# Kernel tuning notes

Measured on AMD Instinct MI355X. Metric: run time of the kernel, lower is better.

The kernel has to match this reference:

```python
import jax, jax.numpy as jnp
import numpy as np

N_OPS = 32
D_REASON = 128
TOP_K = 2
EPS = 1e-05
LEAK = 1e-05  # coefficient on the all-ops leak term


def setup_inputs() -> dict:
    key = jax.random.key(0)
    k1, k2, k3, k4 = jax.random.split(key, 4)
    B, S = 8, 2048
    x = jax.random.normal(k1, (B, S, D_REASON), dtype=jnp.float32)
    indices = jax.random.randint(k2, (B, S, TOP_K), 0, N_OPS, dtype=jnp.int64)
    weights = jax.random.uniform(k3, (B, S, TOP_K), dtype=jnp.float32)
    ops = 0.02 * jax.random.normal(k4, (N_OPS, D_REASON, D_REASON), dtype=jnp.float32)
    return {"x": x, "indices": indices, "weights": weights, "ops": ops}


def _ternary_effective(ops):
    # scale_n = clamp(mean|W_n|, 1e-5); q = STE ternary quantize; W_eff = q * scale
    scale = jnp.maximum(jnp.mean(jnp.abs(ops), axis=(1, 2)), EPS)  # (N,)
    q_hard = jnp.clip(jnp.round(ops / scale[:, None, None]), -1.0, 1.0)
    # STE: identity gradient w.r.t. ops through the quantizer
    q = ops + jax.lax.stop_gradient(q_hard - ops)
    return q * scale[:, None, None]  # (N, D, D)


def reference(x, indices, weights, ops):
    # x: (B,S,D); indices: (B,S,K) int; weights: (B,S,K); ops: (N,D,D)
    w_eff = _ternary_effective(ops)  # (N, D_out, D_in)
    # F.linear(x, W) = x @ W.T, for every op at once -> T: (B,S,N,D_out)
    T = jnp.einsum("bsd,nod->bsno", x, w_eff)
    total = T.sum(axis=2)  # sum over all ops, (B,S,D)
    # gather the selected top_k ops per token: (B,S,K,D)
    gathered = jnp.take_along_axis(T, indices[..., None].astype(jnp.int32), axis=2)
    routed = jnp.sum(weights[..., None] * gathered, axis=2)  # (B,S,D)
    return LEAK * total / N_OPS + routed
```

## Files before the change

kernel.cpp:

```cpp
#include <hip/hip_runtime.h>

#define N_OPS 32
#define D 128
#define MAT (D * D)
#define EPS 1e-5f
#define NTOK (8 * 2048)
#define NASSIGN (NTOK * 2)
#define CAP 40960
#define EXP_BLKS (CAP / 256)

typedef __attribute__((ext_vector_type(8))) short short8;
typedef __attribute__((ext_vector_type(4))) float f32x4;

__device__ inline unsigned short f2bf(float f) {
    unsigned int u = __float_as_uint(f);
    return (unsigned short)((u + 0x7FFF + ((u >> 16) & 1)) >> 16);
}
__device__ inline float bf2f(unsigned short h) {
    return __uint_as_float(((unsigned int)h) << 16);
}

__global__ __launch_bounds__(256) void k_prep(const float* __restrict__ ops,
                                              const int* __restrict__ idx,
                                              const float* __restrict__ x,
                                              float* __restrict__ scale,
                                              int* __restrict__ hist2,
                                              unsigned short* __restrict__ xb,
                                              unsigned short* __restrict__ wb) {
    if (blockIdx.x < N_OPS) {
        const int e = blockIdx.x;
        const float* W = ops + e * MAT;
        float s = 0.f;
        for (int i = threadIdx.x; i < MAT; i += 256) s += fabsf(W[i]);
        for (int off = 32; off; off >>= 1) s += __shfl_xor(s, off);
        __shared__ float red[4];
        __shared__ float s_scale;
        const int lane = threadIdx.x & 63, wid = threadIdx.x >> 6;
        if (lane == 0) red[wid] = s;
        __syncthreads();
        if (threadIdx.x == 0) {
            s_scale = fmaxf((red[0] + red[1] + red[2] + red[3]) / (float)MAT, EPS);
            scale[e] = s_scale;
        }
        __syncthreads();
        const float sc = s_scale;
#pragma unroll
        for (int it = 0; it < 8; ++it) {
            const int f = it * 256 + threadIdx.x;
            const int o = f >> 4, dc = f & 15;
            const float4* wp = (const float4*)(W + o * D + dc * 8);
            float4 a = wp[0], b = wp[1];
            float v[8] = {a.x, a.y, a.z, a.w, b.x, b.y, b.z, b.w};
            unsigned short q[8];
#pragma unroll
            for (int j = 0; j < 8; ++j) {
                float t = rintf(v[j] / sc);
                t = fminf(1.f, fmaxf(-1.f, t));
                q[j] = (t == 0.f) ? 0 : (t > 0.f ? 0x3F80 : 0xBF80);
            }
            ((short8*)wb)[e * 2048 + dc * 128 + o] = *(const short8*)q;
        }
    } else if (blockIdx.x < 64) {
        const int b = blockIdx.x - N_OPS;
        __shared__ int lh[N_OPS];
        if (threadIdx.x < N_OPS) lh[threadIdx.x] = 0;
        __syncthreads();
#pragma unroll
        for (int j = 0; j < 4; ++j)
            atomicAdd(&lh[idx[b * 1024 + j * 256 + threadIdx.x]], 1);
        __syncthreads();
        if (threadIdx.x < N_OPS) hist2[b * N_OPS + threadIdx.x] = lh[threadIdx.x];
    } else {
        const int gid = (blockIdx.x - 64) * 256 + threadIdx.x;
        const float4* xp = (const float4*)(x + (size_t)gid * 8);
        float4 a = xp[0], b = xp[1];
        unsigned short o[8] = {f2bf(a.x), f2bf(a.y), f2bf(a.z), f2bf(a.w),
                               f2bf(b.x), f2bf(b.y), f2bf(b.z), f2bf(b.w)};
        ((short8*)xb)[gid] = *(const short8*)o;
    }
}

__global__ __launch_bounds__(256) void k_scatter(const int* __restrict__ idx,
                                                 const int* __restrict__ hist2,
                                                 int* __restrict__ list,
                                                 int* __restrict__ slot_of) {
    const int b = blockIdx.x;
    __shared__ int hl[1024];
    __shared__ int stot[N_OPS];
    __shared__ int soff[N_OPS + 1];
    __shared__ int sbase[N_OPS];
    __shared__ int lh[N_OPS];
    for (int i = threadIdx.x; i < 1024; i += 256) hl[i] = hist2[i];
    if (threadIdx.x < N_OPS) lh[threadIdx.x] = 0;
    __syncthreads();
    if (threadIdx.x < N_OPS) {
        int t = 0;
        for (int b2 = 0; b2 < 32; ++b2) t += hl[b2 * N_OPS + threadIdx.x];
        stot[threadIdx.x] = t;
    }
    __syncthreads();
    if (threadIdx.x == 0) {
        int run = 0;
        for (int e = 0; e < N_OPS; ++e) { soff[e] = run; run += (stot[e] + 255) & ~255; }
        soff[N_OPS] = run;
    }
    __syncthreads();
    if (threadIdx.x < N_OPS) {
        const int e = threadIdx.x;
        int r = soff[e];
        for (int b2 = 0; b2 < b; ++b2) r += hl[b2 * N_OPS + e];
        sbase[e] = r;
    }
    __syncthreads();
#pragma unroll
    for (int j = 0; j < 4; ++j) {
        const int a = b * 1024 + j * 256 + threadIdx.x;
        const int e = idx[a];
        const int r = atomicAdd(&lh[e], 1);
        const int slot = sbase[e] + r;
        list[slot] = (e << 20) | a;
        slot_of[a] = slot;
    }
    for (int s = soff[b] + stot[b] + (int)threadIdx.x; s < soff[b + 1]; s += 256)
        list[s] = -1;
    if (b == 0)
        for (int s = soff[N_OPS] + (int)threadIdx.x; s < CAP; s += 256) list[s] = -1;
}

__global__ __launch_bounds__(256, 2) void k_mfma(const unsigned short* __restrict__ xb,
                                                 const int* __restrict__ list,
                                                 const unsigned short* __restrict__ wb,
                                                 const float* __restrict__ scale,
                                                 unsigned short* __restrict__ partial) {
    __shared__ short8 lB[2048];
    const int lane = threadIdx.x & 63;
    const int wv   = threadIdx.x >> 6;
    const int quad = lane >> 4;
    const int ncol = lane & 15;

    const int base = blockIdx.x * 256;
    const int v0 = list[base];
    if (v0 < 0) return;
    const int e = v0 >> 20;
    const short8* src = (const short8*)wb + e * 2048;
    const float sc = scale[e];

    for (int i = threadIdx.x; i < 2048; i += 256) lB[i] = src[i];
    __syncthreads();

    for (int g = 0; g < 4; ++g) {
        const int rowbase = base + g * 64 + wv * 16;
        const int v = list[rowbase + ncol];
        const int tok = (v < 0) ? 0 : ((v & 0xFFFFF) >> 1);
        const short8* Ap = (const short8*)(xb + (size_t)tok * D);

        f32x4 acc[8];
#pragma unroll
        for (int j = 0; j < 8; ++j) acc[j] = (f32x4){0.f, 0.f, 0.f, 0.f};

#pragma unroll
        for (int s = 0; s < 4; ++s) {
            const short8 a = Ap[s * 4 + quad];
            const short8* Bp = lB + (s * 4 + quad) * 128;
#pragma unroll
            for (int nt = 0; nt < 8; ++nt) {
                const short8 b = Bp[nt * 16 + ncol];
                acc[nt] = __builtin_amdgcn_mfma_f32_16x16x32_bf16(a, b, acc[nt], 0, 0, 0);
            }
        }
#pragma unroll
        for (int nt = 0; nt < 8; ++nt)
#pragma unroll
            for (int r = 0; r < 4; ++r)
                partial[(size_t)(rowbase + quad * 4 + r) * D + nt * 16 + ncol] =
                    f2bf(acc[nt][r] * sc);
    }
}

__global__ __launch_bounds__(256) void k_final(const unsigned short* __restrict__ partial,
                                               const int* __restrict__ slot_of,
                                               const float* __restrict__ wts,
                                               float* __restrict__ out) {
    const int lane = threadIdx.x & 63;
#pragma unroll
    for (int it = 0; it < 8; ++it) {
        const int t = __builtin_amdgcn_readfirstlane(
            blockIdx.x * 32 + it * 4 + (threadIdx.x >> 6));
        const int s0 = slot_of[2 * t], s1 = slot_of[2 * t + 1];
        const float w0 = wts[2 * t], w1 = wts[2 * t + 1];
        const unsigned int a0 = ((const unsigned int*)(partial + (size_t)s0 * D))[lane];
        const unsigned int a1 = ((const unsigned int*)(partial + (size_t)s1 * D))[lane];
        float2 o;
        o.x = w0 * bf2f((unsigned short)(a0 & 0xFFFF))
            + w1 * bf2f((unsigned short)(a1 & 0xFFFF));
        o.y = w0 * bf2f((unsigned short)(a0 >> 16))
            + w1 * bf2f((unsigned short)(a1 >> 16));
        ((float2*)out)[(size_t)t * 64 + lane] = o;
    }
}

extern "C" void kernel_launch(void* const* d_in, const int* in_sizes, int n_in,
                              void* d_out, int out_size, void* d_ws, size_t ws_size,
                              hipStream_t stream) {
    const float* x   = (const float*)d_in[0];
    const int*   idx = (const int*)  d_in[1];
    const float* wts = (const float*)d_in[2];
    const float* ops = (const float*)d_in[3];
    float* out = (float*)d_out;

    unsigned short* partial = (unsigned short*)d_ws;
    unsigned short* xb      = partial + (size_t)CAP * D;
    unsigned short* wb      = xb + (size_t)NTOK * D;
    float*          scale   = (float*)(wb + N_OPS * MAT);
    int*            hist2   = (int*)(scale + 32);
    int*            list    = hist2 + 1024;
    int*            slot_of = list + CAP;

    k_prep<<<1088, 256, 0, stream>>>(ops, idx, x, scale, hist2, xb, wb);
    k_scatter<<<32, 256, 0, stream>>>(idx, hist2, list, slot_of);
    k_mfma<<<EXP_BLKS, 256, 0, stream>>>(xb, list, wb, scale, partial);
    k_final<<<NTOK / 32, 256, 0, stream>>>(partial, slot_of, wts, out);
}
```

Baseline: 104.0 us.

## Fuse x bf16 conversion into MFMA and scatter partials by assignment index

Drops the separate pass that converts x to bf16 in k_prep. k_mfma now reads fp32 x rows directly and converts them in registers. k_mfma also writes each result row to a buffer indexed by assignment id rather than by slot, which removes the slot_of array so k_final reads contiguous rows. The aim is to save the x round-trip through memory and the indirection, at the cost of doubled x read bytes in the GEMM and scattered partial writes.

```diff
diff --git a/kernel.cpp b/kernel.cpp
--- a/kernel.cpp
+++ b/kernel.cpp
@@ -22,10 +22,8 @@
 
 __global__ __launch_bounds__(256) void k_prep(const float* __restrict__ ops,
                                               const int* __restrict__ idx,
-                                              const float* __restrict__ x,
                                               float* __restrict__ scale,
                                               int* __restrict__ hist2,
-                                              unsigned short* __restrict__ xb,
                                               unsigned short* __restrict__ wb) {
     if (blockIdx.x < N_OPS) {
         const int e = blockIdx.x;
@@ -60,7 +58,7 @@
             }
             ((short8*)wb)[e * 2048 + dc * 128 + o] = *(const short8*)q;
         }
-    } else if (blockIdx.x < 64) {
+    } else {
         const int b = blockIdx.x - N_OPS;
         __shared__ int lh[N_OPS];
         if (threadIdx.x < N_OPS) lh[threadIdx.x] = 0;
@@ -70,20 +68,12 @@
             atomicAdd(&lh[idx[b * 1024 + j * 256 + threadIdx.x]], 1);
         __syncthreads();
         if (threadIdx.x < N_OPS) hist2[b * N_OPS + threadIdx.x] = lh[threadIdx.x];
-    } else {
-        const int gid = (blockIdx.x - 64) * 256 + threadIdx.x;
-        const float4* xp = (const float4*)(x + (size_t)gid * 8);
-        float4 a = xp[0], b = xp[1];
-        unsigned short o[8] = {f2bf(a.x), f2bf(a.y), f2bf(a.z), f2bf(a.w),
-                               f2bf(b.x), f2bf(b.y), f2bf(b.z), f2bf(b.w)};
-        ((short8*)xb)[gid] = *(const short8*)o;
     }
 }
 
 __global__ __launch_bounds__(256) void k_scatter(const int* __restrict__ idx,
                                                  const int* __restrict__ hist2,
-                                                 int* __restrict__ list,
-                                                 int* __restrict__ slot_of) {
+                                                 int* __restrict__ list) {
     const int b = blockIdx.x;
     __shared__ int hl[1024];
     __shared__ int stot[N_OPS];
@@ -117,9 +107,7 @@
         const int a = b * 1024 + j * 256 + threadIdx.x;
         const int e = idx[a];
         const int r = atomicAdd(&lh[e], 1);
-        const int slot = sbase[e] + r;
-        list[slot] = (e << 20) | a;
-        slot_of[a] = slot;
+        list[sbase[e] + r] = (e << 20) | a;
     }
     for (int s = soff[b] + stot[b] + (int)threadIdx.x; s < soff[b + 1]; s += 256)
         list[s] = -1;
@@ -127,11 +115,11 @@
         for (int s = soff[N_OPS] + (int)threadIdx.x; s < CAP; s += 256) list[s] = -1;
 }
 
-__global__ __launch_bounds__(256, 2) void k_mfma(const unsigned short* __restrict__ xb,
+__global__ __launch_bounds__(256, 2) void k_mfma(const float* __restrict__ x,
                                                  const int* __restrict__ list,
                                                  const unsigned short* __restrict__ wb,
                                                  const float* __restrict__ scale,
-                                                 unsigned short* __restrict__ partial) {
+                                                 unsigned short* __restrict__ part2) {
     __shared__ short8 lB[2048];
     const int lane = threadIdx.x & 63;
     const int wv   = threadIdx.x >> 6;
@@ -152,7 +140,7 @@
         const int rowbase = base + g * 64 + wv * 16;
         const int v = list[rowbase + ncol];
         const int tok = (v < 0) ? 0 : ((v & 0xFFFFF) >> 1);
-        const short8* Ap = (const short8*)(xb + (size_t)tok * D);
+        const float4* Xp = (const float4*)(x + (size_t)tok * D);
 
         f32x4 acc[8];
 #pragma unroll
@@ -160,7 +148,11 @@
 
 #pragma unroll
         for (int s = 0; s < 4; ++s) {
-            const short8 a = Ap[s * 4 + quad];
+            const float4 xa = Xp[(s * 32 + quad * 8) >> 2];
+            const float4 xb4 = Xp[((s * 32 + quad * 8) >> 2) + 1];
+            unsigned short af[8] = {f2bf(xa.x), f2bf(xa.y), f2bf(xa.z), f2bf(xa.w),
+                                    f2bf(xb4.x), f2bf(xb4.y), f2bf(xb4.z), f2bf(xb4.w)};
+            const short8 a = *(const short8*)af;
             const short8* Bp = lB + (s * 4 + quad) * 128;
 #pragma unroll
             for (int nt = 0; nt < 8; ++nt) {
@@ -169,16 +161,18 @@
             }
         }
 #pragma unroll
-        for (int nt = 0; nt < 8; ++nt)
-#pragma unroll
-            for (int r = 0; r < 4; ++r)
-                partial[(size_t)(rowbase + quad * 4 + r) * D + nt * 16 + ncol] =
-                    f2bf(acc[nt][r] * sc);
-    }
-}
-
-__global__ __launch_bounds__(256) void k_final(const unsigned short* __restrict__ partial,
-                                               const int* __restrict__ slot_of,
+        for (int r = 0; r < 4; ++r) {
+            const int vr = list[rowbase + quad * 4 + r];
+            if (vr < 0) continue;
+            unsigned short* dst = part2 + (size_t)(vr & 0xFFFFF) * D;
+#pragma unroll
+            for (int nt = 0; nt < 8; ++nt)
+                dst[nt * 16 + ncol] = f2bf(acc[nt][r] * sc);
+        }
+    }
+}
+
+__global__ __launch_bounds__(256) void k_final(const unsigned short* __restrict__ part2,
                                                const float* __restrict__ wts,
                                                float* __restrict__ out) {
     const int lane = threadIdx.x & 63;
@@ -186,10 +180,9 @@
     for (int it = 0; it < 8; ++it) {
         const int t = __builtin_amdgcn_readfirstlane(
             blockIdx.x * 32 + it * 4 + (threadIdx.x >> 6));
-        const int s0 = slot_of[2 * t], s1 = slot_of[2 * t + 1];
         const float w0 = wts[2 * t], w1 = wts[2 * t + 1];
-        const unsigned int a0 = ((const unsigned int*)(partial + (size_t)s0 * D))[lane];
-        const unsigned int a1 = ((const unsigned int*)(partial + (size_t)s1 * D))[lane];
+        const unsigned int a0 = ((const unsigned int*)(part2 + (size_t)(2 * t) * D))[lane];
+        const unsigned int a1 = ((const unsigned int*)(part2 + (size_t)(2 * t + 1) * D))[lane];
         float2 o;
         o.x = w0 * bf2f((unsigned short)(a0 & 0xFFFF))
             + w1 * bf2f((unsigned short)(a1 & 0xFFFF));
@@ -208,16 +201,14 @@
     const float* ops = (const float*)d_in[3];
     float* out = (float*)d_out;
 
-    unsigned short* partial = (unsigned short*)d_ws;
-    unsigned short* xb      = partial + (size_t)CAP * D;
-    unsigned short* wb      = xb + (size_t)NTOK * D;
-    float*          scale   = (float*)(wb + N_OPS * MAT);
-    int*            hist2   = (int*)(scale + 32);
-    int*            list    = hist2 + 1024;
-    int*            slot_of = list + CAP;
-
-    k_prep<<<1088, 256, 0, stream>>>(ops, idx, x, scale, hist2, xb, wb);
-    k_scatter<<<32, 256, 0, stream>>>(idx, hist2, list, slot_of);
-    k_mfma<<<EXP_BLKS, 256, 0, stream>>>(xb, list, wb, scale, partial);
-    k_final<<<NTOK / 32, 256, 0, stream>>>(partial, slot_of, wts, out);
-}
+    unsigned short* part2 = (unsigned short*)d_ws;
+    unsigned short* wb    = part2 + (size_t)NASSIGN * D;
+    float*          scale = (float*)(wb + N_OPS * MAT);
+    int*            hist2 = (int*)(scale + 32);
+    int*            list  = hist2 + 1024;
+
+    k_prep<<<64, 256, 0, stream>>>(ops, idx, scale, hist2, wb);
+    k_scatter<<<32, 256, 0, stream>>>(idx, hist2, list);
+    k_mfma<<<EXP_BLKS, 256, 0, stream>>>(x, list, wb, scale, part2);
+    k_final<<<NTOK / 32, 256, 0, stream>>>(part2, wts, out);
+}
```

After: 106.0 us. No clear change (+1.9%).
